# Kernel tuning notes

Measured on AMD Instinct MI355X. Metric: run time of the kernel, lower is better.

Reference implementation:

```python
import jax, jax.numpy as jnp
import numpy as np

N = 100000   # nodes
E = 1600000  # edges (avg degree 16)
D = 64       # input_dim = hidden_dim = output_dim
BN_EPS = 1e-5
LEAKY_SLOPE = 0.01


def setup_inputs() -> dict:
    key = jax.random.key(0)
    ks = jax.random.split(key, 8)
    s = 1.0 / np.sqrt(D)
    return {
        "x": jax.random.normal(ks[0], (N, D), jnp.float32),
        "edge_index": jax.random.randint(ks[1], (2, E), 0, N, dtype=jnp.int32),
        "W1": jax.random.uniform(ks[2], (D, D), jnp.float32, -s, s),
        "b1": jnp.zeros((D,), jnp.float32),
        "gamma": jnp.ones((D,), jnp.float32),
        "beta": jnp.zeros((D,), jnp.float32),
        "W2": jax.random.uniform(ks[3], (D, D), jnp.float32, -s, s),
        "b2": jnp.zeros((D,), jnp.float32),
    }


def reference(x, edge_index, W1, b1, gamma, beta, W2, b2):
    n = x.shape[0]
    # GCN: add self-loops, symmetric normalization D^-1/2 (A+I) D^-1/2
    loops = jnp.arange(n, dtype=edge_index.dtype)
    src = jnp.concatenate([edge_index[0], loops])
    dst = jnp.concatenate([edge_index[1], loops])
    deg = jax.ops.segment_sum(jnp.ones_like(dst, dtype=x.dtype), dst, num_segments=n)
    dinv = jnp.where(deg > 0, jax.lax.rsqrt(jnp.maximum(deg, 1.0)), 0.0)
    norm = dinv[src] * dinv[dst]  # [E+N]

    def gcn(h, W, b):
        h = h @ W                              # [N, D]
        msg = h[src] * norm[:, None]           # gather + scale, [E+N, D]
        return jax.ops.segment_sum(msg, dst, num_segments=n) + b

    h = gcn(x, W1, b1)
    # BatchNorm1d (training-mode batch stats, biased variance)
    mu = jnp.mean(h, axis=0)
    var = jnp.mean((h - mu) ** 2, axis=0)
    h = gamma * (h - mu) * jax.lax.rsqrt(var + BN_EPS) + beta
    # LeakyReLU; dropout p=0.0 is identity
    h = jnp.where(h >= 0, h, LEAKY_SLOPE * h)
    return gcn(h, W2, b2)
```

## Files before the change

kernel.cpp:

```cpp
#include <hip/hip_runtime.h>
#include <hip/hip_fp16.h>

#define LEAKY 0.01f
#define BN_EPS 1e-5f
#define NB 256
#define NW 256
#define EMAX 7168
#define BCAP 12288

typedef int v4i __attribute__((ext_vector_type(4)));

__global__ __launch_bounds__(256) void k_part(const int* __restrict__ src,
                                              const int* __restrict__ dst,
                                              unsigned* __restrict__ barr,
                                              int* __restrict__ bofs,
                                              double* __restrict__ st,
                                              int e, int nper) {
  __shared__ int lcnt[NB], lofs[NB], lcur[NB], sd[256];
  int wb = blockIdx.x, t = threadIdx.x;
  if (wb == 0 && t < 128) st[t] = 0.0;
  int S = (e + NW - 1) / NW;
  int s0 = wb * S, s1 = min(e, s0 + S);
  lcnt[t] = 0;
  lcur[t] = 0;
  __syncthreads();
  for (int i = s0 + t; i < s1; i += 256) atomicAdd(&lcnt[dst[i] / nper], 1);
  __syncthreads();
  int v = lcnt[t];
  sd[t] = v;
  __syncthreads();
  for (int off = 1; off < 256; off <<= 1) {
    int x = (t >= off) ? sd[t - off] : 0;
    __syncthreads();
    sd[t] += x;
    __syncthreads();
  }
  lofs[t] = sd[t] - v;
  bofs[wb * (NB + 1) + t] = sd[t] - v;
  if (t == 255) bofs[wb * (NB + 1) + NB] = sd[255];
  __syncthreads();
  for (int i = s0 + t; i < s1; i += 256) {
    int d = dst[i];
    int b = d / nper;
    int r = atomicAdd(&lcur[b], 1);
    barr[s0 + lofs[b] + r] = ((unsigned)src[i] << 9) | (unsigned)(d - b * nper);
  }
}

__global__ __launch_bounds__(256) void k_csrb(const unsigned* __restrict__ barr,
                                              const int* __restrict__ bofs,
                                              int* __restrict__ csr,
                                              int2* __restrict__ seg2,
                                              float* __restrict__ dinv,
                                              unsigned* __restrict__ Asent,
                                              int n, int nper, int e) {
  __shared__ int eds[EMAX];
  __shared__ int cnt_[512];
  __shared__ int base_[512];
  __shared__ int sd[256];
  __shared__ int ssz[256], soff[256], sstart[256];
  int b = blockIdx.x, t = threadIdx.x;
  if (b == 0 && t < 32) Asent[t] = 0u;
  int S = (e + NW - 1) / NW;
  int lo = b * nper;
  int nn = min(nper, n - lo);
  if (nn < 0) nn = 0;
  int st_ = bofs[t * (NB + 1) + b];
  int en_ = bofs[t * (NB + 1) + b + 1];
  int v = en_ - st_;
  sstart[t] = st_;
  ssz[t] = v;
  sd[t] = v;
  __syncthreads();
  for (int off = 1; off < 256; off <<= 1) {
    int x = (t >= off) ? sd[t - off] : 0;
    __syncthreads();
    sd[t] += x;
    __syncthreads();
  }
  soff[t] = sd[t] - v;
  __syncthreads();
  int total = min(sd[255], EMAX);
  int wv = t >> 6, lane = t & 63;
  int half = lane >> 5, l32 = lane & 31;
  for (int wb = wv * 2 + half; wb < NW; wb += 8) {
    int sz = ssz[wb], of = soff[wb];
    const unsigned* rp = barr + (size_t)wb * S + sstart[wb];
    for (int k = l32; k < sz && of + k < EMAX; k += 32) eds[of + k] = (int)rp[k];
  }
  cnt_[t] = 0;
  cnt_[t + 256] = 0;
  __syncthreads();
  for (int i = t; i < total; i += 256) atomicAdd(&cnt_[eds[i] & 511], 1);
  __syncthreads();
  int c0 = cnt_[2 * t], c1 = cnt_[2 * t + 1];
  int p0 = (2 * t < nn) ? ((c0 + 15) & ~15) : 0;
  int p1 = (2 * t + 1 < nn) ? ((c1 + 15) & ~15) : 0;
  int ts = p0 + p1;
  sd[t] = ts;
  __syncthreads();
  for (int off = 1; off < 256; off <<= 1) {
    int x = (t >= off) ? sd[t - off] : 0;
    __syncthreads();
    sd[t] += x;
    __syncthreads();
  }
  int run = sd[t] - ts;
  base_[2 * t] = run;
  base_[2 * t + 1] = run + p0;
  __syncthreads();
  int bb = b * BCAP;
  for (int i = t; i < nn; i += 256) {
    int c = cnt_[i];
    int pc = (c + 15) & ~15;
    int ba = bb + base_[i];
    seg2[lo + i] = make_int2(ba, ba + pc);
    dinv[lo + i] = rsqrtf((float)(c + 1));
    for (int j = c; j < pc; j++) csr[ba + j] = n;
  }
  __syncthreads();
  cnt_[t] = 0;
  cnt_[t + 256] = 0;
  __syncthreads();
  for (int i = t; i < total; i += 256) {
    int vv = eds[i];
    int lcl = vv & 511;
    int r = atomicAdd(&cnt_[lcl], 1);
    csr[bb + base_[lcl] + r] = vv >> 9;
  }
  if (b == 0 && t == 0) dinv[n] = 0.f;
}

template <bool BN>
__global__ __launch_bounds__(256) void k_gemm(const void* __restrict__ Xv,
                                              const float* __restrict__ W,
                                              __half* __restrict__ Y, int n,
                                              const float* __restrict__ dinv,
                                              const double* __restrict__ st,
                                              const float* __restrict__ gamma,
                                              const float* __restrict__ beta) {
  __shared__ float Ws[64][68];
  __shared__ float Xs[64][68];
  __shared__ float smu[64], sisd[64];
  int t = threadIdx.x;
  if (BN) {
    if (t < 64) {
      double mu = st[t] / n;
      double var = st[64 + t] / n - mu * mu;
      smu[t] = (float)mu;
      sisd[t] = (float)(1.0 / sqrt(var + (double)BN_EPS));
    }
    __syncthreads();
  }
  int rowbase = blockIdx.x * 64;
#pragma unroll
  for (int p = 0; p < 4; p++) {
    int idx = (p * 256 + t) * 4;
    *(float4*)&Ws[idx >> 6][idx & 63] = *(const float4*)&W[idx];
  }
  if (BN) {
    const __half* Xh = (const __half*)Xv;
#pragma unroll
    for (int p = 0; p < 2; p++) {
      int idx = (p * 256 + t) * 8;
      int r = idx >> 6, c = idx & 63;
      int gr = rowbase + r;
      float vp[8];
      if (gr < n) {
        int4 hv = *(const int4*)&Xh[(size_t)gr * 64 + c];
        __half2* hp = (__half2*)&hv;
#pragma unroll
        for (int q = 0; q < 4; q++) {
          float2 f = __half22float2(hp[q]);
          vp[2 * q] = f.x;
          vp[2 * q + 1] = f.y;
        }
      } else {
#pragma unroll
        for (int q = 0; q < 8; q++) vp[q] = 0.f;
      }
#pragma unroll
      for (int q = 0; q < 8; q++) {
        float z = gamma[c + q] * (vp[q] - smu[c + q]) * sisd[c + q] + beta[c + q];
        Xs[r][c + q] = (z >= 0.f) ? z : LEAKY * z;
      }
    }
  } else {
    const float* X = (const float*)Xv;
#pragma unroll
    for (int p = 0; p < 4; p++) {
      int idx = (p * 256 + t) * 4;
      int r = idx >> 6, c = idx & 63;
      int gr = rowbase + r;
      float4 v = (gr < n) ? *(const float4*)&X[(size_t)gr * 64 + c]
                          : make_float4(0.f, 0.f, 0.f, 0.f);
      *(float4*)&Xs[r][c] = v;
    }
  }
  __syncthreads();
  int r = t >> 2;
  int cq = t & 3;
  float acc[16];
#pragma unroll
  for (int j = 0; j < 16; j++) acc[j] = 0.f;
#pragma unroll 4
  for (int k = 0; k < 64; k++) {
    float xv = Xs[r][k];
#pragma unroll
    for (int j = 0; j < 16; j++) acc[j] += xv * Ws[k][cq * 16 + j];
  }
  int gr = rowbase + r;
  if (gr < n) {
    float dv = dinv[gr];
    __half2 h2[8];
#pragma unroll
    for (int j = 0; j < 8; j++)
      h2[j] = __floats2half2_rn(acc[2 * j] * dv, acc[2 * j + 1] * dv);
    __half* yp = &Y[(size_t)gr * 64 + cq * 16];
    *(int4*)yp = *(int4*)&h2[0];
    *(int4*)(yp + 8) = *(int4*)&h2[4];
  }
}

template <bool FP16OUT>
__global__ __launch_bounds__(256) void k_agg(const __half* __restrict__ H,
                                             void* __restrict__ Optr,
                                             const int2* __restrict__ seg2,
                                             const int* __restrict__ csr,
                                             const float* __restrict__ dinv,
                                             const float* __restrict__ bias, int n) {
  int wave = (blockIdx.x * 256 + threadIdx.x) >> 6;
  int lane = threadIdx.x & 63;
  int i = wave;
  if (i >= n) return;
  float di = dinv[i];
  int2 sg = seg2[i];
  int s0 = sg.x, s1 = sg.y;
  int m = lane & 31;
  bool loA = lane < 32;
  float2 sf = __half22float2(*(const __half2*)&H[(size_t)i * 64 + 2 * m]);
  float a0 = loA ? sf.x : 0.f;
  float a1 = loA ? sf.y : 0.f;
  const v4i* cp = (const v4i*)csr;
  int j = s0 >> 2, jend = s1 >> 2;
  v4i q0 = cp[j];
  v4i q1 = cp[j + 1];
  v4i q2 = cp[j + 2];
  v4i q3 = cp[j + 3];
  for (; j < jend; j += 4) {
    v4i p0 = cp[j + 4];
    v4i p1 = cp[j + 5];
    v4i p2 = cp[j + 6];
    v4i p3 = cp[j + 7];
    int i0 = loA ? q0[0] : q0[1];
    int i1 = loA ? q0[2] : q0[3];
    int i2 = loA ? q1[0] : q1[1];
    int i3 = loA ? q1[2] : q1[3];
    int i4 = loA ? q2[0] : q2[1];
    int i5 = loA ? q2[2] : q2[3];
    int i6 = loA ? q3[0] : q3[1];
    int i7 = loA ? q3[2] : q3[3];
    float2 f0 = __half22float2(*(const __half2*)&H[(size_t)i0 * 64 + 2 * m]);
    float2 f1 = __half22float2(*(const __half2*)&H[(size_t)i1 * 64 + 2 * m]);
    float2 f2 = __half22float2(*(const __half2*)&H[(size_t)i2 * 64 + 2 * m]);
    float2 f3 = __half22float2(*(const __half2*)&H[(size_t)i3 * 64 + 2 * m]);
    float2 f4 = __half22float2(*(const __half2*)&H[(size_t)i4 * 64 + 2 * m]);
    float2 f5 = __half22float2(*(const __half2*)&H[(size_t)i5 * 64 + 2 * m]);
    float2 f6 = __half22float2(*(const __half2*)&H[(size_t)i6 * 64 + 2 * m]);
    float2 f7 = __half22float2(*(const __half2*)&H[(size_t)i7 * 64 + 2 * m]);
    a0 += f0.x + f1.x + f2.x + f3.x;
    a1 += f0.y + f1.y + f2.y + f3.y;
    a0 += f4.x + f5.x + f6.x + f7.x;
    a1 += f4.y + f5.y + f6.y + f7.y;
    q0 = p0;
    q1 = p1;
    q2 = p2;
    q3 = p3;
  }
  a0 += __shfl_xor(a0, 32, 64);
  a1 += __shfl_xor(a1, 32, 64);
  if (loA) {
    float2 bv = *(const float2*)&bias[2 * m];
    float o0 = di * a0 + bv.x;
    float o1 = di * a1 + bv.y;
    if constexpr (FP16OUT) {
      ((__half2*)Optr)[(size_t)i * 32 + m] = __floats2half2_rn(o0, o1);
    } else {
      float2 o;
      o.x = o0;
      o.y = o1;
      *(float2*)&((float*)Optr)[(size_t)i * 64 + 2 * m] = o;
    }
  }
}

__global__ __launch_bounds__(256) void k_bnstats(const __half* __restrict__ H,
                                                 double* __restrict__ st, int n) {
  __shared__ double ds0[8][32], ds1[8][32], dq0[8][32], dq1[8][32];
  int t = threadIdx.x;
  int m = t & 31;
  int g = t >> 5;
  double s0 = 0.0, s1 = 0.0, q0 = 0.0, q1 = 0.0;
  const __half2* H2 = (const __half2*)H;
  for (int r = blockIdx.x * 8 + g; r < n; r += gridDim.x * 8) {
    float2 f = __half22float2(H2[(size_t)r * 32 + m]);
    s0 += f.x;
    s1 += f.y;
    q0 += (double)f.x * f.x;
    q1 += (double)f.y * f.y;
  }
  ds0[g][m] = s0;
  ds1[g][m] = s1;
  dq0[g][m] = q0;
  dq1[g][m] = q1;
  __syncthreads();
  if (g == 0) {
    double a0 = 0, a1 = 0, b0 = 0, b1 = 0;
#pragma unroll
    for (int j = 0; j < 8; j++) {
      a0 += ds0[j][m];
      a1 += ds1[j][m];
      b0 += dq0[j][m];
      b1 += dq1[j][m];
    }
    atomicAdd(&st[2 * m], a0);
    atomicAdd(&st[2 * m + 1], a1);
    atomicAdd(&st[64 + 2 * m], b0);
    atomicAdd(&st[64 + 2 * m + 1], b1);
  }
}

extern "C" void kernel_launch(void* const* d_in, const int* in_sizes, int n_in,
                              void* d_out, int out_size, void* d_ws, size_t ws_size,
                              hipStream_t stream) {
  const float* x     = (const float*)d_in[0];
  const int*   ei    = (const int*)d_in[1];
  const float* W1    = (const float*)d_in[2];
  const float* b1    = (const float*)d_in[3];
  const float* gamma = (const float*)d_in[4];
  const float* beta  = (const float*)d_in[5];
  const float* W2    = (const float*)d_in[6];
  const float* b2    = (const float*)d_in[7];
  float* out = (float*)d_out;

  int n = in_sizes[0] / 64;
  int e = in_sizes[1] / 2;
  const int* srcv = ei;
  const int* dstv = ei + e;
  int nper = (n + NB - 1) / NB;

  char* ws = (char*)d_ws;
  size_t p = 0;
  auto alloc = [&](size_t bytes) {
    void* r = ws + p;
    p += (bytes + 255) & ~(size_t)255;
    return r;
  };
  unsigned* barr = (unsigned*)alloc((size_t)(e + 256) * 4);
  int*      bofs = (int*)alloc((size_t)NW * (NB + 1) * 4);
  int*      csr  = (int*)alloc(((size_t)NB * BCAP + 256) * 4);
  int2*     seg2 = (int2*)alloc((size_t)n * 8);
  float*    dinv = (float*)alloc((size_t)(n + 1) * 4);
  double*   st   = (double*)alloc(128 * 8);
  __half*   A    = (__half*)alloc((size_t)(n + 1) * 64 * 2);
  __half*   B    = (__half*)alloc((size_t)n * 64 * 2);

  int gG = (n + 63) / 64;
  int gAgg = (n + 3) / 4;

  k_part<<<NW, 256, 0, stream>>>(srcv, dstv, barr, bofs, st, e, nper);
  k_csrb<<<NB, 256, 0, stream>>>(barr, bofs, csr, seg2, dinv,
                                 (unsigned*)(A + (size_t)n * 64), n, nper, e);

  k_gemm<false><<<gG, 256, 0, stream>>>(x, W1, A, n, dinv, nullptr, nullptr, nullptr);
  k_agg<true><<<gAgg, 256, 0, stream>>>(A, B, seg2, csr, dinv, b1, n);
  k_bnstats<<<256, 256, 0, stream>>>(B, st, n);
  k_gemm<true><<<gG, 256, 0, stream>>>(B, W2, A, n, dinv, st, gamma, beta);
  k_agg<false><<<gAgg, 256, 0, stream>>>(A, out, seg2, csr, dinv, b2, n);
}
```

Before: 203.0 us.

## Merge CSR build with first GEMM and apply source normalization in aggregation

The CSR-building kernel and the first-layer GEMM are merged into one launch. The first NB blocks build the CSR and the remaining blocks compute x@W1 without the dinv prescale, so the two independent stages run concurrently and one kernel launch is removed. Because the GEMM no longer has dinv available, the first aggregation loads dinv per neighbor and weights each gathered row by it. That adds eight scalar gathers per unrolled iteration, and the padding entries rely on dinv[n] being zero.

```diff
diff --git a/kernel.cpp b/kernel.cpp
--- a/kernel.cpp
+++ b/kernel.cpp
@@ -47,155 +47,183 @@
   }
 }
 
-__global__ __launch_bounds__(256) void k_csrb(const unsigned* __restrict__ barr,
-                                              const int* __restrict__ bofs,
-                                              int* __restrict__ csr,
-                                              int2* __restrict__ seg2,
-                                              float* __restrict__ dinv,
-                                              unsigned* __restrict__ Asent,
-                                              int n, int nper, int e) {
-  __shared__ int eds[EMAX];
-  __shared__ int cnt_[512];
-  __shared__ int base_[512];
-  __shared__ int sd[256];
-  __shared__ int ssz[256], soff[256], sstart[256];
-  int b = blockIdx.x, t = threadIdx.x;
-  if (b == 0 && t < 32) Asent[t] = 0u;
-  int S = (e + NW - 1) / NW;
-  int lo = b * nper;
-  int nn = min(nper, n - lo);
-  if (nn < 0) nn = 0;
-  int st_ = bofs[t * (NB + 1) + b];
-  int en_ = bofs[t * (NB + 1) + b + 1];
-  int v = en_ - st_;
-  sstart[t] = st_;
-  ssz[t] = v;
-  sd[t] = v;
-  __syncthreads();
-  for (int off = 1; off < 256; off <<= 1) {
-    int x = (t >= off) ? sd[t - off] : 0;
-    __syncthreads();
-    sd[t] += x;
-    __syncthreads();
-  }
-  soff[t] = sd[t] - v;
-  __syncthreads();
-  int total = min(sd[255], EMAX);
-  int wv = t >> 6, lane = t & 63;
-  int half = lane >> 5, l32 = lane & 31;
-  for (int wb = wv * 2 + half; wb < NW; wb += 8) {
-    int sz = ssz[wb], of = soff[wb];
-    const unsigned* rp = barr + (size_t)wb * S + sstart[wb];
-    for (int k = l32; k < sz && of + k < EMAX; k += 32) eds[of + k] = (int)rp[k];
-  }
-  cnt_[t] = 0;
-  cnt_[t + 256] = 0;
-  __syncthreads();
-  for (int i = t; i < total; i += 256) atomicAdd(&cnt_[eds[i] & 511], 1);
-  __syncthreads();
-  int c0 = cnt_[2 * t], c1 = cnt_[2 * t + 1];
-  int p0 = (2 * t < nn) ? ((c0 + 15) & ~15) : 0;
-  int p1 = (2 * t + 1 < nn) ? ((c1 + 15) & ~15) : 0;
-  int ts = p0 + p1;
-  sd[t] = ts;
-  __syncthreads();
-  for (int off = 1; off < 256; off <<= 1) {
-    int x = (t >= off) ? sd[t - off] : 0;
-    __syncthreads();
-    sd[t] += x;
-    __syncthreads();
-  }
-  int run = sd[t] - ts;
-  base_[2 * t] = run;
-  base_[2 * t + 1] = run + p0;
-  __syncthreads();
-  int bb = b * BCAP;
-  for (int i = t; i < nn; i += 256) {
-    int c = cnt_[i];
-    int pc = (c + 15) & ~15;
-    int ba = bb + base_[i];
-    seg2[lo + i] = make_int2(ba, ba + pc);
-    dinv[lo + i] = rsqrtf((float)(c + 1));
-    for (int j = c; j < pc; j++) csr[ba + j] = n;
-  }
-  __syncthreads();
-  cnt_[t] = 0;
-  cnt_[t + 256] = 0;
-  __syncthreads();
-  for (int i = t; i < total; i += 256) {
-    int vv = eds[i];
-    int lcl = vv & 511;
-    int r = atomicAdd(&cnt_[lcl], 1);
-    csr[bb + base_[lcl] + r] = vv >> 9;
-  }
-  if (b == 0 && t == 0) dinv[n] = 0.f;
-}
-
-template <bool BN>
-__global__ __launch_bounds__(256) void k_gemm(const void* __restrict__ Xv,
-                                              const float* __restrict__ W,
-                                              __half* __restrict__ Y, int n,
-                                              const float* __restrict__ dinv,
-                                              const double* __restrict__ st,
-                                              const float* __restrict__ gamma,
-                                              const float* __restrict__ beta) {
-  __shared__ float Ws[64][68];
-  __shared__ float Xs[64][68];
-  __shared__ float smu[64], sisd[64];
+__global__ __launch_bounds__(256) void k_mid(const unsigned* __restrict__ barr,
+                                             const int* __restrict__ bofs,
+                                             int* __restrict__ csr,
+                                             int2* __restrict__ seg2,
+                                             float* __restrict__ dinv,
+                                             unsigned* __restrict__ Asent,
+                                             int n, int nper, int e,
+                                             const float* __restrict__ X,
+                                             const float* __restrict__ W,
+                                             __half* __restrict__ Y) {
+  __shared__ __align__(16) int smem_i[9216];
   int t = threadIdx.x;
-  if (BN) {
-    if (t < 64) {
-      double mu = st[t] / n;
-      double var = st[64 + t] / n - mu * mu;
-      smu[t] = (float)mu;
-      sisd[t] = (float)(1.0 / sqrt(var + (double)BN_EPS));
-    }
-    __syncthreads();
-  }
-  int rowbase = blockIdx.x * 64;
-#pragma unroll
-  for (int p = 0; p < 4; p++) {
-    int idx = (p * 256 + t) * 4;
-    *(float4*)&Ws[idx >> 6][idx & 63] = *(const float4*)&W[idx];
-  }
-  if (BN) {
-    const __half* Xh = (const __half*)Xv;
-#pragma unroll
-    for (int p = 0; p < 2; p++) {
-      int idx = (p * 256 + t) * 8;
-      int r = idx >> 6, c = idx & 63;
-      int gr = rowbase + r;
-      float vp[8];
-      if (gr < n) {
-        int4 hv = *(const int4*)&Xh[(size_t)gr * 64 + c];
-        __half2* hp = (__half2*)&hv;
-#pragma unroll
-        for (int q = 0; q < 4; q++) {
-          float2 f = __half22float2(hp[q]);
-          vp[2 * q] = f.x;
-          vp[2 * q + 1] = f.y;
-        }
-      } else {
-#pragma unroll
-        for (int q = 0; q < 8; q++) vp[q] = 0.f;
-      }
-#pragma unroll
-      for (int q = 0; q < 8; q++) {
-        float z = gamma[c + q] * (vp[q] - smu[c + q]) * sisd[c + q] + beta[c + q];
-        Xs[r][c + q] = (z >= 0.f) ? z : LEAKY * z;
-      }
-    }
+  if (blockIdx.x < NB) {
+    int* eds    = smem_i;
+    int* cnt_   = smem_i + 7168;
+    int* base_  = smem_i + 7680;
+    int* sd     = smem_i + 8192;
+    int* ssz    = smem_i + 8448;
+    int* soff   = smem_i + 8704;
+    int* sstart = smem_i + 8960;
+    int b = blockIdx.x;
+    if (b == 0 && t < 32) Asent[t] = 0u;
+    int S = (e + NW - 1) / NW;
+    int lo = b * nper;
+    int nn = min(nper, n - lo);
+    if (nn < 0) nn = 0;
+    int st_ = bofs[t * (NB + 1) + b];
+    int en_ = bofs[t * (NB + 1) + b + 1];
+    int v = en_ - st_;
+    sstart[t] = st_;
+    ssz[t] = v;
+    sd[t] = v;
+    __syncthreads();
+    for (int off = 1; off < 256; off <<= 1) {
+      int x = (t >= off) ? sd[t - off] : 0;
+      __syncthreads();
+      sd[t] += x;
+      __syncthreads();
+    }
+    soff[t] = sd[t] - v;
+    __syncthreads();
+    int total = min(sd[255], EMAX);
+    int wv = t >> 6, lane = t & 63;
+    int half = lane >> 5, l32 = lane & 31;
+    for (int wb = wv * 2 + half; wb < NW; wb += 8) {
+      int sz = ssz[wb], of = soff[wb];
+      const unsigned* rp = barr + (size_t)wb * S + sstart[wb];
+      for (int k = l32; k < sz && of + k < EMAX; k += 32) eds[of + k] = (int)rp[k];
+    }
+    cnt_[t] = 0;
+    cnt_[t + 256] = 0;
+    __syncthreads();
+    for (int i = t; i < total; i += 256) atomicAdd(&cnt_[eds[i] & 511], 1);
+    __syncthreads();
+    int c0 = cnt_[2 * t], c1 = cnt_[2 * t + 1];
+    int p0 = (2 * t < nn) ? ((c0 + 15) & ~15) : 0;
+    int p1 = (2 * t + 1 < nn) ? ((c1 + 15) & ~15) : 0;
+    int ts = p0 + p1;
+    sd[t] = ts;
+    __syncthreads();
+    for (int off = 1; off < 256; off <<= 1) {
+      int x = (t >= off) ? sd[t - off] : 0;
+      __syncthreads();
+      sd[t] += x;
+      __syncthreads();
+    }
+    int run = sd[t] - ts;
+    base_[2 * t] = run;
+    base_[2 * t + 1] = run + p0;
+    __syncthreads();
+    int bb = b * BCAP;
+    for (int i = t; i < nn; i += 256) {
+      int c = cnt_[i];
+      int pc = (c + 15) & ~15;
+      int ba = bb + base_[i];
+      seg2[lo + i] = make_int2(ba, ba + pc);
+      dinv[lo + i] = rsqrtf((float)(c + 1));
+      for (int j = c; j < pc; j++) csr[ba + j] = n;
+    }
+    __syncthreads();
+    cnt_[t] = 0;
+    cnt_[t + 256] = 0;
+    __syncthreads();
+    for (int i = t; i < total; i += 256) {
+      int vv = eds[i];
+      int lcl = vv & 511;
+      int r = atomicAdd(&cnt_[lcl], 1);
+      csr[bb + base_[lcl] + r] = vv >> 9;
+    }
+    if (b == 0 && t == 0) dinv[n] = 0.f;
   } else {
-    const float* X = (const float*)Xv;
+    float(*Ws)[68] = (float(*)[68])smem_i;
+    float(*Xs)[68] = (float(*)[68])(smem_i + 4352);
+    int rowbase = (blockIdx.x - NB) * 64;
 #pragma unroll
     for (int p = 0; p < 4; p++) {
       int idx = (p * 256 + t) * 4;
+      *(float4*)&Ws[idx >> 6][idx & 63] = *(const float4*)&W[idx];
       int r = idx >> 6, c = idx & 63;
       int gr = rowbase + r;
       float4 v = (gr < n) ? *(const float4*)&X[(size_t)gr * 64 + c]
                           : make_float4(0.f, 0.f, 0.f, 0.f);
       *(float4*)&Xs[r][c] = v;
     }
+    __syncthreads();
+    int r = t >> 2;
+    int cq = t & 3;
+    float acc[16];
+#pragma unroll
+    for (int j = 0; j < 16; j++) acc[j] = 0.f;
+#pragma unroll 4
+    for (int k = 0; k < 64; k++) {
+      float xv = Xs[r][k];
+#pragma unroll
+      for (int j = 0; j < 16; j++) acc[j] += xv * Ws[k][cq * 16 + j];
+    }
+    int gr = rowbase + r;
+    if (gr < n) {
+      __half2 h2[8];
+#pragma unroll
+      for (int j = 0; j < 8; j++)
+        h2[j] = __floats2half2_rn(acc[2 * j], acc[2 * j + 1]);
+      __half* yp = &Y[(size_t)gr * 64 + cq * 16];
+      *(int4*)yp = *(int4*)&h2[0];
+      *(int4*)(yp + 8) = *(int4*)&h2[4];
+    }
+  }
+}
+
+__global__ __launch_bounds__(256) void k_gemm2(const __half* __restrict__ Xh,
+                                               const float* __restrict__ W,
+                                               __half* __restrict__ Y, int n,
+                                               const float* __restrict__ dinv,
+                                               const double* __restrict__ st,
+                                               const float* __restrict__ gamma,
+                                               const float* __restrict__ beta) {
+  __shared__ float Ws[64][68];
+  __shared__ float Xs[64][68];
+  __shared__ float smu[64], sisd[64];
+  int t = threadIdx.x;
+  if (t < 64) {
+    double mu = st[t] / n;
+    double var = st[64 + t] / n - mu * mu;
+    smu[t] = (float)mu;
+    sisd[t] = (float)(1.0 / sqrt(var + (double)BN_EPS));
+  }
+  __syncthreads();
+  int rowbase = blockIdx.x * 64;
+#pragma unroll
+  for (int p = 0; p < 4; p++) {
+    int idx = (p * 256 + t) * 4;
+    *(float4*)&Ws[idx >> 6][idx & 63] = *(const float4*)&W[idx];
+  }
+#pragma unroll
+  for (int p = 0; p < 2; p++) {
+    int idx = (p * 256 + t) * 8;
+    int r = idx >> 6, c = idx & 63;
+    int gr = rowbase + r;
+    float vp[8];
+    if (gr < n) {
+      int4 hv = *(const int4*)&Xh[(size_t)gr * 64 + c];
+      __half2* hp = (__half2*)&hv;
+#pragma unroll
+      for (int q = 0; q < 4; q++) {
+        float2 f = __half22float2(hp[q]);
+        vp[2 * q] = f.x;
+        vp[2 * q + 1] = f.y;
+      }
+    } else {
+#pragma unroll
+      for (int q = 0; q < 8; q++) vp[q] = 0.f;
+    }
+#pragma unroll
+    for (int q = 0; q < 8; q++) {
+      float z = gamma[c + q] * (vp[q] - smu[c + q]) * sisd[c + q] + beta[c + q];
+      Xs[r][c + q] = (z >= 0.f) ? z : LEAKY * z;
+    }
   }
   __syncthreads();
   int r = t >> 2;
@@ -222,7 +250,7 @@
   }
 }
 
-template <bool FP16OUT>
+template <bool WEIGHTED, bool FP16OUT>
 __global__ __launch_bounds__(256) void k_agg(const __half* __restrict__ H,
                                              void* __restrict__ Optr,
                                              const int2* __restrict__ seg2,
@@ -239,8 +267,9 @@
   int m = lane & 31;
   bool loA = lane < 32;
   float2 sf = __half22float2(*(const __half2*)&H[(size_t)i * 64 + 2 * m]);
-  float a0 = loA ? sf.x : 0.f;
-  float a1 = loA ? sf.y : 0.f;
+  float sw = WEIGHTED ? di : 1.f;
+  float a0 = loA ? sf.x * sw : 0.f;
+  float a1 = loA ? sf.y * sw : 0.f;
   const v4i* cp = (const v4i*)csr;
   int j = s0 >> 2, jend = s1 >> 2;
   v4i q0 = cp[j];
@@ -268,10 +297,19 @@
     float2 f5 = __half22float2(*(const __half2*)&H[(size_t)i5 * 64 + 2 * m]);
     float2 f6 = __half22float2(*(const __half2*)&H[(size_t)i6 * 64 + 2 * m]);
     float2 f7 = __half22float2(*(const __half2*)&H[(size_t)i7 * 64 + 2 * m]);
-    a0 += f0.x + f1.x + f2.x + f3.x;
-    a1 += f0.y + f1.y + f2.y + f3.y;
-    a0 += f4.x + f5.x + f6.x + f7.x;
-    a1 += f4.y + f5.y + f6.y + f7.y;
+    if constexpr (WEIGHTED) {
+      float w0 = dinv[i0], w1 = dinv[i1], w2 = dinv[i2], w3 = dinv[i3];
+      float w4 = dinv[i4], w5 = dinv[i5], w6 = dinv[i6], w7 = dinv[i7];
+      a0 += f0.x * w0 + f1.x * w1 + f2.x * w2 + f3.x * w3;
+      a1 += f0.y * w0 + f1.y * w1 + f2.y * w2 + f3.y * w3;
+      a0 += f4.x * w4 + f5.x * w5 + f6.x * w6 + f7.x * w7;
+      a1 += f4.y * w4 + f5.y * w5 + f6.y * w6 + f7.y * w7;
+    } else {
+      a0 += f0.x + f1.x + f2.x + f3.x;
+      a1 += f0.y + f1.y + f2.y + f3.y;
+      a0 += f4.x + f5.x + f6.x + f7.x;
+      a1 += f4.y + f5.y + f6.y + f7.y;
+    }
     q0 = p0;
     q1 = p1;
     q2 = p2;
@@ -369,12 +407,11 @@
   int gAgg = (n + 3) / 4;
 
   k_part<<<NW, 256, 0, stream>>>(srcv, dstv, barr, bofs, st, e, nper);
-  k_csrb<<<NB, 256, 0, stream>>>(barr, bofs, csr, seg2, dinv,
-                                 (unsigned*)(A + (size_t)n * 64), n, nper, e);
-
-  k_gemm<false><<<gG, 256, 0, stream>>>(x, W1, A, n, dinv, nullptr, nullptr, nullptr);
-  k_agg<true><<<gAgg, 256, 0, stream>>>(A, B, seg2, csr, dinv, b1, n);
+  k_mid<<<NB + gG, 256, 0, stream>>>(barr, bofs, csr, seg2, dinv,
+                                     (unsigned*)(A + (size_t)n * 64), n, nper, e,
+                                     x, W1, A);
+  k_agg<true, true><<<gAgg, 256, 0, stream>>>(A, B, seg2, csr, dinv, b1, n);
   k_bnstats<<<256, 256, 0, stream>>>(B, st, n);
-  k_gemm<true><<<gG, 256, 0, stream>>>(B, W2, A, n, dinv, st, gamma, beta);
-  k_agg<false><<<gAgg, 256, 0, stream>>>(A, out, seg2, csr, dinv, b2, n);
-}
+  k_gemm2<<<gG, 256, 0, stream>>>(B, W2, A, n, dinv, st, gamma, beta);
+  k_agg<false, false><<<gAgg, 256, 0, stream>>>(A, out, seg2, csr, dinv, b2, n);
+}
```

Measured after the change: 190.2 us. 6.3% less time.
